# Kernel tuning notes

Hardware: AMD Instinct MI355X
Metric: run time of the kernel (lower is better)

## Reference

```python
import jax, jax.numpy as jnp
import numpy as np

N_NODES = 100000


def _gcn_layer(x, edge_index, W, b):
    # x: [N, Fin], edge_index: [2, E]
    row, col = edge_index[0], edge_index[1]
    n = x.shape[0]
    ones = jnp.ones(row.shape[0], dtype=x.dtype)
    deg = jax.ops.segment_sum(ones, row, num_segments=n)  # bincount(row)
    deg_inv_sqrt = jnp.where(deg > 0, deg ** -0.5, 0.0).astype(x.dtype)
    norm = deg_inv_sqrt[row] * deg_inv_sqrt[col]  # [E]
    h = x @ W + b  # linear first, as in the torch code
    # sparse COO matmul == scatter-add of norm-scaled source features into row
    msgs = norm[:, None] * h[col]  # [E, Fout]
    return jax.ops.segment_sum(msgs, row, num_segments=n)


def setup_inputs() -> dict:
    key = jax.random.key(0)
    ks = jax.random.split(key, 7)
    N, Fin, H, Fout = N_NODES, 256, 64, 64
    Epos, Eneg = 1600000, 1600000
    x = jax.random.normal(ks[0], (N, Fin), dtype=jnp.float32)
    pos_edge_index = jax.random.randint(ks[1], (2, Epos), 0, N, dtype=jnp.int64)
    neg_edge_index = jax.random.randint(ks[2], (2, Eneg), 0, N, dtype=jnp.int64)
    W1 = jax.random.normal(ks[3], (Fin, H), dtype=jnp.float32) * (1.0 / np.sqrt(Fin))
    b1 = jax.random.normal(ks[4], (H,), dtype=jnp.float32) * 0.01
    W2 = jax.random.normal(ks[5], (H, Fout), dtype=jnp.float32) * (1.0 / np.sqrt(H))
    b2 = jax.random.normal(ks[6], (Fout,), dtype=jnp.float32) * 0.01
    return {"x": x, "pos_edge_index": pos_edge_index, "neg_edge_index": neg_edge_index,
            "W1": W1, "b1": b1, "W2": W2, "b2": b2}


def reference(x, pos_edge_index, neg_edge_index, W1, b1, W2, b2):
    # encode: two GCN layers over pos_edge_index.
    # Note: the original calls self.PairNorm(x) but discards the result,
    # so PairNorm has no effect on the output.
    h = jax.nn.relu(_gcn_layer(x, pos_edge_index, W1, b1))
    z = _gcn_layer(h, pos_edge_index, W2, b2)  # [N, 64]
    # decode: dot product over concatenated pos+neg edges
    edge = jnp.concatenate([pos_edge_index, neg_edge_index], axis=-1)  # [2, Ep+En]
    return jnp.sum(z[edge[0]] * z[edge[1]], axis=-1)  # [Ep+En]
```

## Files before the change

kernel.cpp:

```cpp
#include <hip/hip_runtime.h>
#include <hip/hip_fp16.h>

#define FIN 256
#define FH  64
#define SCAN_BLK 1024
#define NCHUNK 8

typedef float f4v __attribute__((ext_vector_type(4)));
typedef float f2v __attribute__((ext_vector_type(2)));


__global__ __launch_bounds__(256) void deg_kernel(const int* __restrict__ rows,
                                                  unsigned* __restrict__ deg, int E) {
    int e = blockIdx.x * 256 + threadIdx.x;
    if (e < E) atomicAdd(&deg[rows[e]], 1u);
}


__global__ __launch_bounds__(256) void scan_block_kernel(const unsigned* __restrict__ deg,
                                                         int* __restrict__ rowptr,
                                                         int* __restrict__ blocksums, int N) {
    __shared__ int wsum[4];
    const int t = threadIdx.x;
    const int base = blockIdx.x * SCAN_BLK + t * 4;
    int d0 = 0, d1 = 0, d2 = 0, d3 = 0;
    if (base + 0 < N) d0 = (int)deg[base + 0];
    if (base + 1 < N) d1 = (int)deg[base + 1];
    if (base + 2 < N) d2 = (int)deg[base + 2];
    if (base + 3 < N) d3 = (int)deg[base + 3];
    const int tot = d0 + d1 + d2 + d3;
    const int lane = t & 63, wv = t >> 6;
    int inc = tot;
#pragma unroll
    for (int off = 1; off < 64; off <<= 1) {
        int v = __shfl_up(inc, off, 64);
        if (lane >= off) inc += v;
    }
    if (lane == 63) wsum[wv] = inc;
    __syncthreads();
    int woff = 0;
    for (int w = 0; w < wv; ++w) woff += wsum[w];
    const int ex = woff + inc - tot;
    if (base + 0 < N) rowptr[base + 0] = ex;
    if (base + 1 < N) rowptr[base + 1] = ex + d0;
    if (base + 2 < N) rowptr[base + 2] = ex + d0 + d1;
    if (base + 3 < N) rowptr[base + 3] = ex + d0 + d1 + d2;
    if (t == 255) blocksums[blockIdx.x] = woff + inc;
}


__global__ __launch_bounds__(256) void scan_add_kernel(int* __restrict__ rowptr,
                                                       int* __restrict__ cursor,
                                                       const unsigned* __restrict__ deg,
                                                       float* __restrict__ dis,
                                                       const int* __restrict__ blocksums,
                                                       int nb, int N, int E) {
    __shared__ int pre;
    const int t = threadIdx.x;
    const int i0 = blockIdx.x * 256;
    const int c0 = i0 / SCAN_BLK;
    if (t == 0) {
        int s = 0;
        for (int k = 0; k < c0; ++k) s += blocksums[k];
        pre = s;
    }
    __syncthreads();
    int i = i0 + t;
    if (i < N) {
        int v = rowptr[i] + pre;
        rowptr[i] = v;
        cursor[i] = v;
        unsigned d = deg[i];
        dis[i] = d ? 1.0f / sqrtf((float)d) : 0.0f;
    }
    if (i == 0) rowptr[N] = E;
}


__global__ __launch_bounds__(256) void scatter_edges_kernel(const int* __restrict__ rows,
                                                            const int* __restrict__ cols,
                                                            int* __restrict__ cursor,
                                                            int* __restrict__ colOut,
                                                            int* __restrict__ inv,
                                                            float chunk_scale, int E) {
    const int chunk = blockIdx.x & (NCHUNK - 1);
    const int eb = blockIdx.x >> 3;
    int e = eb * 256 + threadIdx.x;
    if (e >= E) return;
    int r = rows[e];
    int rc = (int)((float)r * chunk_scale);
    rc = rc > (NCHUNK - 1) ? (NCHUNK - 1) : rc;
    if (rc == chunk) {
        int p = atomicAdd(&cursor[r], 1);
        colOut[p] = cols[e];
        inv[e] = p;
    }
}


__global__ __launch_bounds__(256) void gemm1_kernel(const float* __restrict__ x,
                                                    const float* __restrict__ W,
                                                    const float* __restrict__ b,
                                                    const float* __restrict__ dis,
                                                    __half2* __restrict__ outh, int N) {
    __shared__ float xs[32][132];
    __shared__ float ws[32][64];
    const int t = threadIdx.x;
    const int rb = blockIdx.x * 128;
    const int rg = t >> 3, cg = t & 7;
    const int r0 = rg * 4, c0 = cg * 8;
    float acc[4][8];
#pragma unroll
    for (int i = 0; i < 4; ++i)
#pragma unroll
        for (int j = 0; j < 8; ++j) acc[i][j] = 0.f;

    const f4v* x4 = (const f4v*)x;
    const int kk = (t & 7) * 4;
    const int rloc = t >> 3;

    for (int k0 = 0; k0 < FIN; k0 += 32) {
        __syncthreads();
        {
            const float4* w4 = (const float4*)(W + k0 * 64);
            float4* wl = (float4*)&ws[0][0];
            wl[t]       = w4[t];
            wl[t + 256] = w4[t + 256];
        }
#pragma unroll
        for (int p = 0; p < 4; ++p) {
            int r = rloc + p * 32;
            int gr = rb + r; if (gr >= N) gr = N - 1;
            f4v v = __builtin_nontemporal_load(&x4[gr * 64 + (k0 >> 2) + (t & 7)]);
            xs[kk + 0][r] = v.x; xs[kk + 1][r] = v.y;
            xs[kk + 2][r] = v.z; xs[kk + 3][r] = v.w;
        }
        __syncthreads();
#pragma unroll
        for (int k = 0; k < 32; ++k) {
            float4 xa = *(const float4*)&xs[k][r0];
            float4 wa = *(const float4*)&ws[k][c0];
            float4 wb = *(const float4*)&ws[k][c0 + 4];
            float xr[4] = {xa.x, xa.y, xa.z, xa.w};
            float wr[8] = {wa.x, wa.y, wa.z, wa.w, wb.x, wb.y, wb.z, wb.w};
#pragma unroll
            for (int i = 0; i < 4; ++i)
#pragma unroll
                for (int j = 0; j < 8; ++j) acc[i][j] = fmaf(xr[i], wr[j], acc[i][j]);
        }
    }
    float bias[8];
#pragma unroll
    for (int j = 0; j < 8; ++j) bias[j] = b[c0 + j];
#pragma unroll
    for (int i = 0; i < 4; ++i) {
        int gr = rb + r0 + i;
        if (gr < N) {
            float d = dis[gr];
            __half2 o[4];
            o[0] = __floats2half2_rn((acc[i][0] + bias[0]) * d, (acc[i][1] + bias[1]) * d);
            o[1] = __floats2half2_rn((acc[i][2] + bias[2]) * d, (acc[i][3] + bias[3]) * d);
            o[2] = __floats2half2_rn((acc[i][4] + bias[4]) * d, (acc[i][5] + bias[5]) * d);
            o[3] = __floats2half2_rn((acc[i][6] + bias[6]) * d, (acc[i][7] + bias[7]) * d);
            *(uint4*)&outh[gr * 32 + (c0 >> 1)] = *(uint4*)o;
        }
    }
}


__global__ __launch_bounds__(256) void gather_agg16_kernel(const int* __restrict__ rowptr,
                                                           const int* __restrict__ cols,
                                                           const __half2* __restrict__ h2v,
                                                           const float* __restrict__ dscale,
                                                           float* __restrict__ outf,
                                                           __half2* __restrict__ outh,
                                                           int N, int tohalf) {
    int r = blockIdx.x * 8 + (threadIdx.x >> 5);
    int l32 = threadIdx.x & 31;
    if (r >= N) return;
    const int rowbase = threadIdx.x & 32;
    int s = rowptr[r], e = rowptr[r + 1];
    float2 acc[8];
#pragma unroll
    for (int u = 0; u < 8; ++u) { acc[u].x = 0.f; acc[u].y = 0.f; }
    for (int base = s; base < e; base += 32) {
        int n = e - base; if (n > 32) n = 32;
        int idx = (l32 < n) ? cols[base + l32] : 0;
        int j = 0;
        for (; j + 15 < n; j += 16) {
            __half2 tv[16];
#pragma unroll
            for (int u = 0; u < 16; ++u) {
                int c = __shfl(idx, rowbase + j + u);
                tv[u] = h2v[(size_t)c * 32 + l32];
            }
#pragma unroll
            for (int u = 0; u < 16; ++u) {
                float2 f = __half22float2(tv[u]);
                acc[u & 7].x += f.x; acc[u & 7].y += f.y;
            }
        }
        for (; j + 3 < n; j += 4) {
            __half2 tv[4];
#pragma unroll
            for (int u = 0; u < 4; ++u) {
                int c = __shfl(idx, rowbase + j + u);
                tv[u] = h2v[(size_t)c * 32 + l32];
            }
#pragma unroll
            for (int u = 0; u < 4; ++u) {
                float2 f = __half22float2(tv[u]);
                acc[u].x += f.x; acc[u].y += f.y;
            }
        }
        for (; j < n; ++j) {
            int c = __shfl(idx, rowbase + j);
            float2 f = __half22float2(h2v[(size_t)c * 32 + l32]);
            acc[0].x += f.x; acc[0].y += f.y;
        }
    }
    float2 v;
    v.x = ((acc[0].x + acc[1].x) + (acc[2].x + acc[3].x)) + ((acc[4].x + acc[5].x) + (acc[6].x + acc[7].x));
    v.y = ((acc[0].y + acc[1].y) + (acc[2].y + acc[3].y)) + ((acc[4].y + acc[5].y) + (acc[6].y + acc[7].y));
    if (dscale) { float d = dscale[r]; v.x *= d; v.y *= d; }
    if (tohalf) {
        outh[(size_t)r * 32 + l32] = __float22half2_rn(v);
    } else {
        f2v o; o.x = v.x; o.y = v.y;
        __builtin_nontemporal_store(o, (f2v*)&outf[(size_t)r * 64 + l32 * 2]);
    }
}


__global__ __launch_bounds__(256) void gemm2_kernel(const float* __restrict__ agg,
                                                    const float* __restrict__ dis,
                                                    const float* __restrict__ W,
                                                    const float* __restrict__ b,
                                                    __half2* __restrict__ outh, int N) {
    __shared__ float xs[64][132];
    __shared__ float ws[64][64];
    const int t = threadIdx.x;
    const int rb = blockIdx.x * 128;
    {
        const float4* w4 = (const float4*)W;
        float4* wl = (float4*)&ws[0][0];
#pragma unroll
        for (int p = 0; p < 4; ++p) wl[p * 256 + t] = w4[p * 256 + t];
    }
    {
        const f4v* a4 = (const f4v*)agg;
        const int c4 = (t & 15) * 4;
        const int rloc = t >> 4;
#pragma unroll
        for (int p = 0; p < 8; ++p) {
            int r = rloc + p * 16;
            int gr = rb + r; if (gr >= N) gr = N - 1;
            float d = dis[gr];
            f4v v = __builtin_nontemporal_load(&a4[gr * 16 + (t & 15)]);
            xs[c4 + 0][r] = fmaxf(v.x * d, 0.f);
            xs[c4 + 1][r] = fmaxf(v.y * d, 0.f);
            xs[c4 + 2][r] = fmaxf(v.z * d, 0.f);
            xs[c4 + 3][r] = fmaxf(v.w * d, 0.f);
        }
    }
    __syncthreads();
    const int rg = t >> 3, cg = t & 7;
    const int r0 = rg * 4, c0 = cg * 8;
    float acc[4][8];
#pragma unroll
    for (int i = 0; i < 4; ++i)
#pragma unroll
        for (int j = 0; j < 8; ++j) acc[i][j] = 0.f;
#pragma unroll 16
    for (int k = 0; k < 64; ++k) {
        float4 xa = *(const float4*)&xs[k][r0];
        float4 wa = *(const float4*)&ws[k][c0];
        float4 wb = *(const float4*)&ws[k][c0 + 4];
        float xr[4] = {xa.x, xa.y, xa.z, xa.w};
        float wr[8] = {wa.x, wa.y, wa.z, wa.w, wb.x, wb.y, wb.z, wb.w};
#pragma unroll
        for (int i = 0; i < 4; ++i)
#pragma unroll
            for (int j = 0; j < 8; ++j) acc[i][j] = fmaf(xr[i], wr[j], acc[i][j]);
    }
    float bias[8];
#pragma unroll
    for (int j = 0; j < 8; ++j) bias[j] = b[c0 + j];
#pragma unroll
    for (int i = 0; i < 4; ++i) {
        int gr = rb + r0 + i;
        if (gr < N) {
            float d = dis[gr];
            __half2 o[4];
            o[0] = __floats2half2_rn((acc[i][0] + bias[0]) * d, (acc[i][1] + bias[1]) * d);
            o[1] = __floats2half2_rn((acc[i][2] + bias[2]) * d, (acc[i][3] + bias[3]) * d);
            o[2] = __floats2half2_rn((acc[i][4] + bias[4]) * d, (acc[i][5] + bias[5]) * d);
            o[3] = __floats2half2_rn((acc[i][6] + bias[6]) * d, (acc[i][7] + bias[7]) * d);
            *(uint4*)&outh[gr * 32 + (c0 >> 1)] = *(uint4*)o;
        }
    }
}


__device__ __forceinline__ float dot8h(float4 A, float4 B) {
    union { float4 f; __half2 h[4]; } ua, ub;
    ua.f = A; ub.f = B;
    float s = 0.f;
#pragma unroll
    for (int k = 0; k < 4; ++k) {
        float2 fa = __half22float2(ua.h[k]);
        float2 fb = __half22float2(ub.h[k]);
        s = fmaf(fa.x, fb.x, s);
        s = fmaf(fa.y, fb.y, s);
    }
    return s;
}

__global__ __launch_bounds__(256) void decode16_kernel(const int* __restrict__ rowptr,
                                                       const int* __restrict__ cols,
                                                       const int* __restrict__ ne,
                                                       const float4* __restrict__ zf4,
                                                       float* __restrict__ P,
                                                       float* __restrict__ outp,
                                                       int N, int negB, int Ep, int En) {
    const int t = threadIdx.x;
    const int l8 = t & 7;

    if ((int)blockIdx.x < negB) {
        const int g = t >> 3;
        const int base = blockIdx.x * 256;
        int a[8], b[8];
        bool v[8];
#pragma unroll
        for (int q = 0; q < 8; ++q) {
            int e = base + q * 32 + g;
            v[q] = e < En;
            a[q] = 0; b[q] = 0;
            if (v[q]) { a[q] = ne[e]; b[q] = ne[En + e]; }
        }
        float4 va[8], vb[8];
#pragma unroll
        for (int q = 0; q < 8; ++q) {
            va[q] = zf4[(size_t)a[q] * 8 + l8];
            vb[q] = zf4[(size_t)b[q] * 8 + l8];
        }
#pragma unroll
        for (int q = 0; q < 8; ++q) {
            float p = dot8h(va[q], vb[q]);
            p += __shfl_xor(p, 4);
            p += __shfl_xor(p, 2);
            p += __shfl_xor(p, 1);
            int e = base + q * 32 + g;
            if (v[q] && l8 == 0) __builtin_nontemporal_store(p, &outp[Ep + e]);
        }
    } else {
        int r = (blockIdx.x - negB) * 8 + (t >> 5);
        if (r >= N) return;
        const int l32 = t & 31;
        const int rowbase = t & 32;
        const int g4 = (t >> 3) & 3;
        int s = rowptr[r], e = rowptr[r + 1];
        if (s == e) return;
        float zr8[8];
        {
            union { float4 f; __half2 h[4]; } uz;
            uz.f = zf4[(size_t)r * 8 + l8];
#pragma unroll
            for (int k = 0; k < 4; ++k) {
                float2 f = __half22float2(uz.h[k]);
                zr8[2 * k] = f.x; zr8[2 * k + 1] = f.y;
            }
        }
        for (int base = s; base < e; base += 32) {
            int n = e - base; if (n > 32) n = 32;
            int idx = (l32 < n) ? cols[base + l32] : 0;
            for (int j = 0; j < n; j += 8) {
                int pos0 = j + g4, pos1 = j + 4 + g4;
                bool a0 = pos0 < n, a1 = pos1 < n;
                int c0 = __shfl(idx, rowbase + (a0 ? pos0 : 0));
                int c1 = __shfl(idx, rowbase + (a1 ? pos1 : 0));
                float4 v0 = zf4[(size_t)c0 * 8 + l8];
                float4 v1 = zf4[(size_t)c1 * 8 + l8];
                union { float4 f; __half2 h[4]; } u0, u1;
                u0.f = v0; u1.f = v1;
                float p0 = 0.f, p1 = 0.f;
#pragma unroll
                for (int k = 0; k < 4; ++k) {
                    float2 f0 = __half22float2(u0.h[k]);
                    float2 f1 = __half22float2(u1.h[k]);
                    p0 = fmaf(zr8[2 * k], f0.x, p0); p0 = fmaf(zr8[2 * k + 1], f0.y, p0);
                    p1 = fmaf(zr8[2 * k], f1.x, p1); p1 = fmaf(zr8[2 * k + 1], f1.y, p1);
                }
                p0 += __shfl_xor(p0, 4); p0 += __shfl_xor(p0, 2); p0 += __shfl_xor(p0, 1);
                p1 += __shfl_xor(p1, 4); p1 += __shfl_xor(p1, 2); p1 += __shfl_xor(p1, 1);
                if (l8 == 0) {
                    if (a0) P[base + pos0] = p0;
                    if (a1) P[base + pos1] = p1;
                }
            }
        }
    }
}


__global__ __launch_bounds__(256) void permute_kernel(const float* __restrict__ P,
                                                      const int* __restrict__ inv,
                                                      float* __restrict__ out, int E) {
    int e = blockIdx.x * 256 + threadIdx.x;
    if (e < E) {
        int p = __builtin_nontemporal_load(&inv[e]);
        __builtin_nontemporal_store(P[p], &out[e]);
    }
}


extern "C" void kernel_launch(void* const* d_in, const int* in_sizes, int n_in,
                              void* d_out, int out_size, void* d_ws, size_t ws_size,
                              hipStream_t stream) {
    const float* x  = (const float*)d_in[0];
    const int*   pe = (const int*)d_in[1];
    const int*   ne = (const int*)d_in[2];
    const float* W1 = (const float*)d_in[3];
    const float* b1 = (const float*)d_in[4];
    const float* W2 = (const float*)d_in[5];
    const float* b2 = (const float*)d_in[6];
    float* outp = (float*)d_out;

    const int N  = in_sizes[0] / FIN;
    const int Ep = in_sizes[1] / 2;
    const int En = in_sizes[2] / 2;

    char* w = (char*)d_ws;
    size_t off = 0;
    auto alloc = [&](size_t bytes) {
        void* p = w + off;
        off = (off + bytes + 255) & ~(size_t)255;
        return p;
    };
    unsigned* deg   = (unsigned*)alloc((size_t)N * 4);
    float* dis      = (float*)alloc((size_t)N * 4);
    int* rowptr     = (int*)alloc((size_t)(N + 1) * 4);
    int* cursor     = (int*)alloc((size_t)N * 4);
    int* blocksums  = (int*)alloc(((size_t)N / SCAN_BLK + 2) * 4);
    int* colsorted  = (int*)alloc((size_t)Ep * 4);
    int* inv        = (int*)alloc((size_t)Ep * 4);
    __half2* A16    = (__half2*)alloc((size_t)N * 64 * 2);
    float* B        = (float*)alloc((size_t)N * 64 * 4);

    const int nscan = (N + SCAN_BLK - 1) / SCAN_BLK;
    const int nEdgeBlocks = (Ep + 255) / 256;

    hipMemsetAsync(deg, 0, (size_t)N * 4, stream);

    deg_kernel<<<nEdgeBlocks, 256, 0, stream>>>(pe, deg, Ep);
    scan_block_kernel<<<nscan, 256, 0, stream>>>(deg, rowptr, blocksums, N);
    scan_add_kernel<<<(N + 255) / 256, 256, 0, stream>>>(rowptr, cursor, deg, dis,
                                                         blocksums, nscan, N, Ep);
    scatter_edges_kernel<<<nEdgeBlocks * NCHUNK, 256, 0, stream>>>(
        pe, pe + Ep, cursor, colsorted, inv, (float)NCHUNK / (float)N, Ep);
    gemm1_kernel<<<(N + 127) / 128, 256, 0, stream>>>(x, W1, b1, dis, A16, N);
    gather_agg16_kernel<<<(N + 7) / 8, 256, 0, stream>>>(rowptr, colsorted, A16, nullptr,
                                                         B, nullptr, N, 0);
    gemm2_kernel<<<(N + 127) / 128, 256, 0, stream>>>(B, dis, W2, b2, A16, N);
    __half2* z16 = (__half2*)B;
    gather_agg16_kernel<<<(N + 7) / 8, 256, 0, stream>>>(rowptr, colsorted, A16, dis,
                                                         nullptr, z16, N, 1);
    float* P = (float*)A16;
    const int negB = (En + 255) / 256;
    const int posB = (N + 7) / 8;
    decode16_kernel<<<negB + posB, 256, 0, stream>>>(rowptr, colsorted, ne,
                                                     (const float4*)z16, P, outp,
                                                     N, negB, Ep, En);
    permute_kernel<<<(Ep + 255) / 256, 256, 0, stream>>>(P, inv, outp, Ep);
}
```

Measured before the change: 531.3 us.

## Fuse layer-1 aggregation with layer-2 GEMM in one gather kernel

Merges the first gather-aggregate and the second dense 64x64 GEMM into one kernel. Each half-wave holds a row's aggregated features in registers, broadcasts them with shuffles and multiplies against W2 staged in shared memory. This drops the fp32 N×64 intermediate buffer write and re-read, plus one kernel launch. The cost is that every gather block now loads W2 into LDS, and the per-row matvec adds shuffle and LDS traffic to a memory-bound kernel.

```diff
diff --git a/kernel.cpp b/kernel.cpp
--- a/kernel.cpp
+++ b/kernel.cpp
@@ -168,17 +168,27 @@
 }
 
 
-__global__ __launch_bounds__(256) void gather_agg16_kernel(const int* __restrict__ rowptr,
-                                                           const int* __restrict__ cols,
-                                                           const __half2* __restrict__ h2v,
-                                                           const float* __restrict__ dscale,
-                                                           float* __restrict__ outf,
-                                                           __half2* __restrict__ outh,
-                                                           int N, int tohalf) {
-    int r = blockIdx.x * 8 + (threadIdx.x >> 5);
-    int l32 = threadIdx.x & 31;
+__global__ __launch_bounds__(256) void gather_mm_kernel(const int* __restrict__ rowptr,
+                                                        const int* __restrict__ cols,
+                                                        const __half2* __restrict__ h2v,
+                                                        const float* __restrict__ dis,
+                                                        const float* __restrict__ W2,
+                                                        const float* __restrict__ b2,
+                                                        __half2* __restrict__ outh, int N) {
+    __shared__ float ws[64][64];
+    const int t = threadIdx.x;
+    {
+        const float4* w4 = (const float4*)W2;
+        float4* wl = (float4*)&ws[0][0];
+#pragma unroll
+        for (int p = 0; p < 4; ++p) wl[p * 256 + t] = w4[p * 256 + t];
+    }
+    __syncthreads();
+
+    int r = blockIdx.x * 8 + (t >> 5);
     if (r >= N) return;
-    const int rowbase = threadIdx.x & 32;
+    const int l32 = t & 31;
+    const int rowbase = t & 32;
     int s = rowptr[r], e = rowptr[r + 1];
     float2 acc[8];
 #pragma unroll
@@ -222,83 +232,80 @@
     float2 v;
     v.x = ((acc[0].x + acc[1].x) + (acc[2].x + acc[3].x)) + ((acc[4].x + acc[5].x) + (acc[6].x + acc[7].x));
     v.y = ((acc[0].y + acc[1].y) + (acc[2].y + acc[3].y)) + ((acc[4].y + acc[5].y) + (acc[6].y + acc[7].y));
-    if (dscale) { float d = dscale[r]; v.x *= d; v.y *= d; }
-    if (tohalf) {
-        outh[(size_t)r * 32 + l32] = __float22half2_rn(v);
-    } else {
-        f2v o; o.x = v.x; o.y = v.y;
-        __builtin_nontemporal_store(o, (f2v*)&outf[(size_t)r * 64 + l32 * 2]);
-    }
-}
-
-
-__global__ __launch_bounds__(256) void gemm2_kernel(const float* __restrict__ agg,
-                                                    const float* __restrict__ dis,
-                                                    const float* __restrict__ W,
-                                                    const float* __restrict__ b,
-                                                    __half2* __restrict__ outh, int N) {
-    __shared__ float xs[64][132];
-    __shared__ float ws[64][64];
-    const int t = threadIdx.x;
-    const int rb = blockIdx.x * 128;
-    {
-        const float4* w4 = (const float4*)W;
-        float4* wl = (float4*)&ws[0][0];
-#pragma unroll
-        for (int p = 0; p < 4; ++p) wl[p * 256 + t] = w4[p * 256 + t];
-    }
-    {
-        const f4v* a4 = (const f4v*)agg;
-        const int c4 = (t & 15) * 4;
-        const int rloc = t >> 4;
-#pragma unroll
-        for (int p = 0; p < 8; ++p) {
-            int r = rloc + p * 16;
-            int gr = rb + r; if (gr >= N) gr = N - 1;
-            float d = dis[gr];
-            f4v v = __builtin_nontemporal_load(&a4[gr * 16 + (t & 15)]);
-            xs[c4 + 0][r] = fmaxf(v.x * d, 0.f);
-            xs[c4 + 1][r] = fmaxf(v.y * d, 0.f);
-            xs[c4 + 2][r] = fmaxf(v.z * d, 0.f);
-            xs[c4 + 3][r] = fmaxf(v.w * d, 0.f);
-        }
-    }
-    __syncthreads();
-    const int rg = t >> 3, cg = t & 7;
-    const int r0 = rg * 4, c0 = cg * 8;
-    float acc[4][8];
-#pragma unroll
-    for (int i = 0; i < 4; ++i)
-#pragma unroll
-        for (int j = 0; j < 8; ++j) acc[i][j] = 0.f;
-#pragma unroll 16
-    for (int k = 0; k < 64; ++k) {
-        float4 xa = *(const float4*)&xs[k][r0];
-        float4 wa = *(const float4*)&ws[k][c0];
-        float4 wb = *(const float4*)&ws[k][c0 + 4];
-        float xr[4] = {xa.x, xa.y, xa.z, xa.w};
-        float wr[8] = {wa.x, wa.y, wa.z, wa.w, wb.x, wb.y, wb.z, wb.w};
-#pragma unroll
-        for (int i = 0; i < 4; ++i)
-#pragma unroll
-            for (int j = 0; j < 8; ++j) acc[i][j] = fmaf(xr[i], wr[j], acc[i][j]);
-    }
-    float bias[8];
-#pragma unroll
-    for (int j = 0; j < 8; ++j) bias[j] = b[c0 + j];
-#pragma unroll
-    for (int i = 0; i < 4; ++i) {
-        int gr = rb + r0 + i;
-        if (gr < N) {
-            float d = dis[gr];
-            __half2 o[4];
-            o[0] = __floats2half2_rn((acc[i][0] + bias[0]) * d, (acc[i][1] + bias[1]) * d);
-            o[1] = __floats2half2_rn((acc[i][2] + bias[2]) * d, (acc[i][3] + bias[3]) * d);
-            o[2] = __floats2half2_rn((acc[i][4] + bias[4]) * d, (acc[i][5] + bias[5]) * d);
-            o[3] = __floats2half2_rn((acc[i][6] + bias[6]) * d, (acc[i][7] + bias[7]) * d);
-            *(uint4*)&outh[gr * 32 + (c0 >> 1)] = *(uint4*)o;
-        }
-    }
+    const float dr = dis[r];
+    v.x = fmaxf(v.x * dr, 0.f);
+    v.y = fmaxf(v.y * dr, 0.f);
+    float2 o; o.x = 0.f; o.y = 0.f;
+#pragma unroll 8
+    for (int kk = 0; kk < 32; ++kk) {
+        float vx = __shfl(v.x, rowbase + kk);
+        float vy = __shfl(v.y, rowbase + kk);
+        float2 w0 = *(const float2*)&ws[2 * kk][2 * l32];
+        float2 w1 = *(const float2*)&ws[2 * kk + 1][2 * l32];
+        o.x = fmaf(vx, w0.x, o.x); o.x = fmaf(vy, w1.x, o.x);
+        o.y = fmaf(vx, w0.y, o.y); o.y = fmaf(vy, w1.y, o.y);
+    }
+    float2 bb = *(const float2*)&b2[2 * l32];
+    o.x = (o.x + bb.x) * dr;
+    o.y = (o.y + bb.y) * dr;
+    outh[(size_t)r * 32 + l32] = __float22half2_rn(o);
+}
+
+
+__global__ __launch_bounds__(256) void gather_z_kernel(const int* __restrict__ rowptr,
+                                                       const int* __restrict__ cols,
+                                                       const __half2* __restrict__ h2v,
+                                                       const float* __restrict__ dscale,
+                                                       __half2* __restrict__ outh, int N) {
+    int r = blockIdx.x * 8 + (threadIdx.x >> 5);
+    int l32 = threadIdx.x & 31;
+    if (r >= N) return;
+    const int rowbase = threadIdx.x & 32;
+    int s = rowptr[r], e = rowptr[r + 1];
+    float2 acc[8];
+#pragma unroll
+    for (int u = 0; u < 8; ++u) { acc[u].x = 0.f; acc[u].y = 0.f; }
+    for (int base = s; base < e; base += 32) {
+        int n = e - base; if (n > 32) n = 32;
+        int idx = (l32 < n) ? cols[base + l32] : 0;
+        int j = 0;
+        for (; j + 15 < n; j += 16) {
+            __half2 tv[16];
+#pragma unroll
+            for (int u = 0; u < 16; ++u) {
+                int c = __shfl(idx, rowbase + j + u);
+                tv[u] = h2v[(size_t)c * 32 + l32];
+            }
+#pragma unroll
+            for (int u = 0; u < 16; ++u) {
+                float2 f = __half22float2(tv[u]);
+                acc[u & 7].x += f.x; acc[u & 7].y += f.y;
+            }
+        }
+        for (; j + 3 < n; j += 4) {
+            __half2 tv[4];
+#pragma unroll
+            for (int u = 0; u < 4; ++u) {
+                int c = __shfl(idx, rowbase + j + u);
+                tv[u] = h2v[(size_t)c * 32 + l32];
+            }
+#pragma unroll
+            for (int u = 0; u < 4; ++u) {
+                float2 f = __half22float2(tv[u]);
+                acc[u].x += f.x; acc[u].y += f.y;
+            }
+        }
+        for (; j < n; ++j) {
+            int c = __shfl(idx, rowbase + j);
+            float2 f = __half22float2(h2v[(size_t)c * 32 + l32]);
+            acc[0].x += f.x; acc[0].y += f.y;
+        }
+    }
+    float2 v;
+    v.x = ((acc[0].x + acc[1].x) + (acc[2].x + acc[3].x)) + ((acc[4].x + acc[5].x) + (acc[6].x + acc[7].x));
+    v.y = ((acc[0].y + acc[1].y) + (acc[2].y + acc[3].y)) + ((acc[4].y + acc[5].y) + (acc[6].y + acc[7].y));
+    float d = dscale[r]; v.x *= d; v.y *= d;
+    outh[(size_t)r * 32 + l32] = __float22half2_rn(v);
 }
 
 
@@ -445,7 +452,8 @@
     int* colsorted  = (int*)alloc((size_t)Ep * 4);
     int* inv        = (int*)alloc((size_t)Ep * 4);
     __half2* A16    = (__half2*)alloc((size_t)N * 64 * 2);
-    float* B        = (float*)alloc((size_t)N * 64 * 4);
+    __half2* B16    = (__half2*)alloc((size_t)N * 64 * 2);
+    float* P        = (float*)alloc((size_t)Ep * 4);
 
     const int nscan = (N + SCAN_BLK - 1) / SCAN_BLK;
     const int nEdgeBlocks = (Ep + 255) / 256;
@@ -459,13 +467,10 @@
     scatter_edges_kernel<<<nEdgeBlocks * NCHUNK, 256, 0, stream>>>(
         pe, pe + Ep, cursor, colsorted, inv, (float)NCHUNK / (float)N, Ep);
     gemm1_kernel<<<(N + 127) / 128, 256, 0, stream>>>(x, W1, b1, dis, A16, N);
-    gather_agg16_kernel<<<(N + 7) / 8, 256, 0, stream>>>(rowptr, colsorted, A16, nullptr,
-                                                         B, nullptr, N, 0);
-    gemm2_kernel<<<(N + 127) / 128, 256, 0, stream>>>(B, dis, W2, b2, A16, N);
-    __half2* z16 = (__half2*)B;
-    gather_agg16_kernel<<<(N + 7) / 8, 256, 0, stream>>>(rowptr, colsorted, A16, dis,
-                                                         nullptr, z16, N, 1);
-    float* P = (float*)A16;
+    gather_mm_kernel<<<(N + 7) / 8, 256, 0, stream>>>(rowptr, colsorted, A16, dis,
+                                                      W2, b2, B16, N);
+    __half2* z16 = A16;
+    gather_z_kernel<<<(N + 7) / 8, 256, 0, stream>>>(rowptr, colsorted, B16, dis, z16, N);
     const int negB = (En + 255) / 256;
     const int posB = (N + 7) / 8;
     decode16_kernel<<<negB + posB, 256, 0, stream>>>(rowptr, colsorted, ne,
```

Result: slower. 552.5 us (+4.0%).
